# Optimization experiments

Measured on AMD Instinct MI355X. Metric: run time of the kernel, lower is better.

## Reference

```python
import jax, jax.numpy as jnp
import numpy as np

B, N, H, STEPS, IN_DIM, OUT_DIM = 512, 81, 128, 16, 10, 9
LN_EPS = 1e-5


def _build_edges():
    # Sudoku constraint graph: edge (j -> i) if cells share row, col, or 3x3 box.
    edges = []
    for i in range(81):
        ri, ci = divmod(i, 9)
        bi = ri // 3 * 3 + ci // 3
        for j in range(81):
            if i == j:
                continue
            rj, cj = divmod(j, 9)
            bj = rj // 3 * 3 + cj // 3
            if ri == rj or ci == cj or bi == bj:
                edges.append((j, i))
    e = np.asarray(edges, dtype=np.int32).T  # [2, 1620]
    return e[0], e[1]


def setup_inputs() -> dict:
    key = jax.random.key(0)
    ks = jax.random.split(key, 24)
    s = 0.02

    def w(k, shape):
        return jax.random.normal(k, shape, dtype=jnp.float32) * s

    src_np, dst_np = _build_edges()
    inp = {
        "x": jax.random.normal(ks[0], (B, N, IN_DIM), dtype=jnp.float32),
        "src": jnp.asarray(src_np),
        "dst": jnp.asarray(dst_np),
        "W_in": w(ks[1], (IN_DIM, H)), "b_in": jnp.zeros((H,), jnp.float32),
        "pos": w(ks[2], (N, H)),
        # message MLP: (2H -> H -> H -> H -> H), ReLU between
        "mW0": w(ks[3], (2 * H, H)), "mb0": jnp.zeros((H,), jnp.float32),
        "mW1": w(ks[4], (H, H)), "mb1": jnp.zeros((H,), jnp.float32),
        "mW2": w(ks[5], (H, H)), "mb2": jnp.zeros((H,), jnp.float32),
        "mW3": w(ks[6], (H, H)), "mb3": jnp.zeros((H,), jnp.float32),
        # node MLP: (3H -> H -> H -> H -> H)
        "nW0": w(ks[7], (3 * H, H)), "nb0": jnp.zeros((H,), jnp.float32),
        "nW1": w(ks[8], (H, H)), "nb1": jnp.zeros((H,), jnp.float32),
        "nW2": w(ks[9], (H, H)), "nb2": jnp.zeros((H,), jnp.float32),
        "nW3": w(ks[10], (H, H)), "nb3": jnp.zeros((H,), jnp.float32),
        "ln_g": jnp.ones((H,), jnp.float32), "ln_b": jnp.zeros((H,), jnp.float32),
        "W_out": w(ks[11], (H, OUT_DIM)), "b_out": jnp.zeros((OUT_DIM,), jnp.float32),
    }
    return inp


def _mlp(x, Ws, bs):
    for W, b in zip(Ws[:-1], bs[:-1]):
        x = jax.nn.relu(x @ W + b)
    return x @ Ws[-1] + bs[-1]


def _layer_norm(h, g, b):
    mu = jnp.mean(h, axis=-1, keepdims=True)
    var = jnp.mean(jnp.square(h - mu), axis=-1, keepdims=True)
    return (h - mu) * jax.lax.rsqrt(var + LN_EPS) * g + b


def reference(x, src, dst, W_in, b_in, pos,
              mW0, mb0, mW1, mb1, mW2, mb2, mW3, mb3,
              nW0, nb0, nW1, nb1, nW2, nb2, nW3, nb3,
              ln_g, ln_b, W_out, b_out):
    mWs, mbs = [mW0, mW1, mW2, mW3], [mb0, mb1, mb2, mb3]
    nWs, nbs = [nW0, nW1, nW2, nW3], [nb0, nb1, nb2, nb3]

    x_embed = x @ W_in + b_in + pos  # [B, N, H]
    h = x_embed
    for _ in range(STEPS):
        h_src = h[:, src]  # [B, E, H] gather
        h_dst = h[:, dst]
        messages = _mlp(jnp.concatenate([h_src, h_dst], axis=-1), mWs, mbs)  # [B, E, H]
        # scatter-add over dst -> [B, N, H]
        aggregated = jnp.zeros_like(h).at[:, dst, :].add(messages)
        h = h + _mlp(jnp.concatenate([h, x_embed, aggregated], axis=-1), nWs, nbs)
        h = _layer_norm(h, ln_g, ln_b)
    return h @ W_out + b_out  # [B, N, 9]
```

## Files before the change

### kernel.cpp

```cpp
#include <hip/hip_runtime.h>
#include <hip/hip_bf16.h>

typedef __bf16 bf16_t;
typedef bf16_t bf16x8 __attribute__((ext_vector_type(8)));
typedef bf16_t bf16x4 __attribute__((ext_vector_type(4)));
typedef float  f32x4  __attribute__((ext_vector_type(4)));
typedef float  f32x16 __attribute__((ext_vector_type(16)));

#define NN   81
#define BB   512
#define BN   41472
#define EE   1620

__device__ __forceinline__ int swz(int r, int k) {
    return (r << 7) + ((((k >> 3) ^ (r & 15)) << 3) | (k & 7));
}

__device__ __forceinline__ int wpack(int n, int k) {
    return ((n >> 6) << 13) + (((((k >> 5) << 2) + ((n >> 4) & 3))) << 9)
         + (((((k >> 3) & 3) << 4) + (n & 15)) << 3) + (k & 7);
}

__device__ __forceinline__ int wpack32(int n, int k) {
    return ((((k >> 4) << 2) | (n >> 5)) << 9)
         + (((((k >> 3) & 1) << 5) | (n & 31)) << 3) + (k & 7);
}

__device__ __forceinline__ unsigned pkbf(float lo, float hi) {
    unsigned a = __float_as_uint(lo) + 0x8000u;
    unsigned b = __float_as_uint(hi) + 0x8000u;
    return __builtin_amdgcn_perm(b, a, 0x07060302);
}

__device__ __forceinline__ unsigned pkbf_t(float lo, float hi) {
    return __builtin_amdgcn_perm(__float_as_uint(hi), __float_as_uint(lo), 0x07060302);
}

__device__ __forceinline__ float bflo(unsigned d) { return __uint_as_float(d << 16); }
__device__ __forceinline__ float bfhi(unsigned d) { return __uint_as_float(d & 0xffff0000u); }

__device__ __forceinline__ unsigned addrelu2(unsigned pd, unsigned qd) {
    float lo = fmaxf(bflo(pd) + bflo(qd), 0.f);
    float hi = fmaxf(bfhi(pd) + bfhi(qd), 0.f);
    return pkbf(lo, hi);
}

__device__ __forceinline__ void gemm128s(f32x4 (&acc)[4][4], const bf16_t* act,
                                         const bf16_t* __restrict__ Wp,
                                         int wm, int wn, int lane, int lrow, int q) {
    f32x4 z = {0.f, 0.f, 0.f, 0.f};
    #pragma unroll
    for (int i = 0; i < 4; i++)
        #pragma unroll
        for (int j = 0; j < 4; j++) acc[i][j] = z;
    const bf16_t* wbase = Wp + (wn << 13) + (lane << 3);
    #pragma unroll
    for (int k0 = 0; k0 < 128; k0 += 32) {
        bf16x8 af[4], wf[4];
        #pragma unroll
        for (int mt = 0; mt < 4; mt++)
            af[mt] = *(const bf16x8*)&act[swz(wm * 64 + mt * 16 + lrow, k0 + q * 8)];
        #pragma unroll
        for (int nt = 0; nt < 4; nt++)
            wf[nt] = *(const bf16x8*)(wbase + ((((k0 >> 5) << 2) + nt) << 9));
        #pragma unroll
        for (int nt = 0; nt < 4; nt++)
            #pragma unroll
            for (int mt = 0; mt < 4; mt++)
                acc[nt][mt] = __builtin_amdgcn_mfma_f32_16x16x32_bf16(wf[nt], af[mt], acc[nt][mt], 0, 0, 0);
    }
}

template<int MT>
__device__ __forceinline__ void gemm_e(f32x16 (&acc)[MT], const bf16_t* act,
                                       const bf16_t* __restrict__ W,
                                       const float* __restrict__ bias,
                                       int wid, int lane) {
    int lm = lane & 31, h = lane >> 5;
    #pragma unroll
    for (int gg = 0; gg < 4; gg++) {
        float4 b4 = *(const float4*)&bias[wid * 32 + 8 * gg + 4 * h];
        #pragma unroll
        for (int mt = 0; mt < MT; mt++) {
            acc[mt][4 * gg + 0] = b4.x; acc[mt][4 * gg + 1] = b4.y;
            acc[mt][4 * gg + 2] = b4.z; acc[mt][4 * gg + 3] = b4.w;
        }
    }
    const bf16_t* wl = W + (lane << 3);
    #pragma unroll
    for (int kk = 0; kk < 8; kk++) {
        bf16x8 wf = *(const bf16x8*)(wl + (((kk << 2) + wid) << 9));
        #pragma unroll
        for (int mt = 0; mt < MT; mt++) {
            bf16x8 af = *(const bf16x8*)&act[swz(mt * 32 + lm, kk * 16 + h * 8)];
            acc[mt] = __builtin_amdgcn_mfma_f32_32x32x16_bf16(wf, af, acc[mt], 0, 0, 0);
        }
    }
}

template<int MT>
__device__ __forceinline__ void wb_e(bf16_t* act, f32x16 (&acc)[MT], int wid, int lane) {
    int lm = lane & 31, h = lane >> 5;
    #pragma unroll
    for (int mt = 0; mt < MT; mt++)
        #pragma unroll
        for (int gg = 0; gg < 4; gg++) {
            int nb = wid * 32 + 8 * gg + 4 * h;
            int m = mt * 32 + lm;
            uint2 u;
            u.x = pkbf_t(fmaxf(acc[mt][4 * gg + 0], 0.f), fmaxf(acc[mt][4 * gg + 1], 0.f));
            u.y = pkbf_t(fmaxf(acc[mt][4 * gg + 2], 0.f), fmaxf(acc[mt][4 * gg + 3], 0.f));
            *(uint2*)&act[swz(m, nb)] = u;
        }
}

__device__ __forceinline__ void gemm32s(f32x4 (&acc)[2][2], const bf16_t* act,
                                        const bf16_t* __restrict__ Wp,
                                        int wid, int lane, int lrow, int q, bool zero) {
    if (zero) {
        f32x4 z = {0.f, 0.f, 0.f, 0.f};
        acc[0][0] = z; acc[0][1] = z; acc[1][0] = z; acc[1][1] = z;
    }
    int wn = wid >> 1, ntb = (wid & 1) << 1;
    const bf16_t* wbase = Wp + (wn << 13) + (lane << 3);
    #pragma unroll
    for (int k0 = 0; k0 < 128; k0 += 32) {
        bf16x8 af[2], wf[2];
        af[0] = *(const bf16x8*)&act[swz(lrow, k0 + q * 8)];
        af[1] = *(const bf16x8*)&act[swz(16 + lrow, k0 + q * 8)];
        wf[0] = *(const bf16x8*)(wbase + ((((k0 >> 5) << 2) + ntb) << 9));
        wf[1] = *(const bf16x8*)(wbase + ((((k0 >> 5) << 2) + ntb + 1) << 9));
        #pragma unroll
        for (int nt = 0; nt < 2; nt++)
            #pragma unroll
            for (int mt = 0; mt < 2; mt++)
                acc[nt][mt] = __builtin_amdgcn_mfma_f32_16x16x32_bf16(wf[nt], af[mt], acc[nt][mt], 0, 0, 0);
    }
}

__device__ __forceinline__ void wb32(bf16_t* act, f32x4 (&acc)[2][2], const float* __restrict__ bias,
                                     int colb, int lrow, int q) {
    #pragma unroll
    for (int nt = 0; nt < 2; nt++) {
        int nb = colb + nt * 16 + q * 4;
        float4 b4 = *(const float4*)&bias[nb];
        #pragma unroll
        for (int mt = 0; mt < 2; mt++) {
            int m = mt * 16 + lrow;
            uint2 u;
            u.x = pkbf_t(fmaxf(acc[nt][mt][0] + b4.x, 0.f), fmaxf(acc[nt][mt][1] + b4.y, 0.f));
            u.y = pkbf_t(fmaxf(acc[nt][mt][2] + b4.z, 0.f), fmaxf(acc[nt][mt][3] + b4.w, 0.f));
            *(uint2*)&act[swz(m, nb)] = u;
        }
    }
}


__global__ __launch_bounds__(256) void k_embed(const float* __restrict__ x, const float* __restrict__ W_in,
                                               const float* __restrict__ b_in, const float* __restrict__ pos,
                                               bf16_t* __restrict__ hb) {
    int idx = blockIdx.x * 256 + threadIdx.x;
    int row = idx >> 7, col = idx & 127;
    int n = row % NN;
    const float* xr = x + (size_t)row * 10;
    float s = b_in[col] + pos[n * 128 + col];
    #pragma unroll
    for (int k = 0; k < 10; k++) s += xr[k] * W_in[k * 128 + col];
    hb[idx] = (bf16_t)s;
}

struct PackArgs { const float* s[9]; };

__global__ __launch_bounds__(256) void k_pack_all(PackArgs pa, bf16_t* __restrict__ dst) {
    const int slot[9] = {0, 1, 2, 3, 4, 6, 7, 8, 9};
    int idx = blockIdx.x * 256 + threadIdx.x;
    int w = idx >> 14, r = idx & 16383;
    int n = r >> 7, k = r & 127;
    int po = (w == 2 || w == 3) ? wpack32(n, k) : wpack(n, k);
    dst[slot[w] * 16384 + po] = (bf16_t)pa.s[w][k * 128 + n];
}

__global__ __launch_bounds__(256) void k_fuse(const float* __restrict__ mW3, const float* __restrict__ nW0,
                                              bf16_t* __restrict__ Ft) {
    int idx = blockIdx.x * 256 + threadIdx.x;
    int n = idx >> 7, k = idx & 127;
    float s = 0.f;
    for (int j = 0; j < 128; j++) s += mW3[k * 128 + j] * nW0[(256 + j) * 128 + n];
    Ft[wpack(n, k)] = (bf16_t)s;
}

__global__ __launch_bounds__(128) void k_bias(const float* __restrict__ nb0, const float* __restrict__ mb3,
                                              const float* __restrict__ nW0, float* __restrict__ bfix) {
    int n = threadIdx.x;
    float s = 0.f;
    for (int j = 0; j < 128; j++) s += mb3[j] * nW0[(256 + j) * 128 + n];
    bfix[n] = nb0[n] + 20.f * s;
}

__global__ __launch_bounds__(256, 2) void k_simple3(const bf16_t* __restrict__ in,
                                                    const bf16_t* __restrict__ Wp,
                                                    const float* __restrict__ bfix,
                                                    const float* __restrict__ mb0,
                                                    bf16_t* __restrict__ C2b,
                                                    bf16_t* __restrict__ Pd,
                                                    bf16_t* __restrict__ Qd) {
    __shared__ __align__(16) bf16_t act[16384];
    int tid = threadIdx.x;
    int sel = blockIdx.x / 324, blk = blockIdx.x - sel * 324;
    size_t i0 = (size_t)blk * 128;
    int lane = tid & 63, wid = tid >> 6;
    int wm = wid >> 1, wn = wid & 1, lrow = lane & 15, q = lane >> 4;

    for (int ch = tid; ch < 2048; ch += 256) {
        int r = ch >> 4, p = ch & 15;
        *(uint4*)&act[swz(r, p << 3)] = *(const uint4*)(in + (i0 + r) * 128 + (p << 3));
    }
    __syncthreads();
    const bf16_t* W = Wp + (sel == 0 ? 9 * 16384 : (sel == 1 ? 0 : 16384));
    f32x4 acc[4][4];
    gemm128s(acc, act, W, wm, wn, lane, lrow, q);
    bf16_t* dst = (sel == 0) ? C2b : ((sel == 1) ? Pd : Qd);
    #pragma unroll
    for (int nt = 0; nt < 4; nt++) {
        int nb = wn * 64 + nt * 16 + q * 4;
        float4 b4 = (sel == 0) ? *(const float4*)&bfix[nb]
                  : (sel == 2) ? *(const float4*)&mb0[nb]
                               : make_float4(0.f, 0.f, 0.f, 0.f);
        #pragma unroll
        for (int mt = 0; mt < 4; mt++) {
            int m = wm * 64 + mt * 16 + lrow;
            uint2 u;
            u.x = pkbf(acc[nt][mt][0] + b4.x, acc[nt][mt][1] + b4.y);
            u.y = pkbf(acc[nt][mt][2] + b4.z, acc[nt][mt][3] + b4.w);
            *(uint2*)(dst + (i0 + m) * 128 + nb) = u;
        }
    }
}

__global__ __launch_bounds__(256, 4) void k_edge(const bf16_t* __restrict__ P, const bf16_t* __restrict__ Q,
                                                 const int* __restrict__ src, const bf16_t* __restrict__ Wp,
                                                 const float* __restrict__ mb1, const float* __restrict__ mb2,
                                                 bf16_t* __restrict__ SA) {
    __shared__ __align__(16) bf16_t act[16384];
    int tid = threadIdx.x;
    int g = blockIdx.x, b = blockIdx.y;
    int e0 = g * 120, n0 = g * 6;
    int nreal = (e0 + 120 <= EE) ? 120 : (EE - e0);
    int lane = tid & 63, w = tid >> 6;

    for (int ch = tid; ch < 2048; ch += 256) {
        int r = ch >> 4, p = ch & 15;
        uint4 o;
        if (r < nreal) {
            int e = e0 + r;
            int sn = src[e];
            int dn = n0 + r / 20;
            uint4 pv = *(const uint4*)(P + (((size_t)b * NN + sn) << 7) + (p << 3));
            uint4 qv = *(const uint4*)(Q + (((size_t)b * NN + dn) << 7) + (p << 3));
            o.x = addrelu2(pv.x, qv.x);
            o.y = addrelu2(pv.y, qv.y);
            o.z = addrelu2(pv.z, qv.z);
            o.w = addrelu2(pv.w, qv.w);
        } else {
            o.x = 0u; o.y = 0u; o.z = 0u; o.w = 0u;
        }
        *(uint4*)&act[swz(r, p << 3)] = o;
    }
    __syncthreads();

    if (nreal == 120) {
        f32x16 acc[4];
        gemm_e<4>(acc, act, Wp + 2 * 16384, mb1, w, lane);
        __syncthreads();
        wb_e<4>(act, acc, w, lane);
        __syncthreads();
        gemm_e<4>(acc, act, Wp + 3 * 16384, mb2, w, lane);
        __syncthreads();
        wb_e<4>(act, acc, w, lane);
        __syncthreads();
    } else {
        f32x16 acc[2];
        gemm_e<2>(acc, act, Wp + 2 * 16384, mb1, w, lane);
        __syncthreads();
        wb_e<2>(act, acc, w, lane);
        __syncthreads();
        gemm_e<2>(acc, act, Wp + 3 * 16384, mb2, w, lane);
        __syncthreads();
        wb_e<2>(act, acc, w, lane);
        __syncthreads();
    }

    if (tid < 192) {
        int j = tid >> 5;
        int sub = tid & 31;
        int rr = sub >> 1;
        int half = sub & 1;
        int nodes = nreal / 20;
        if (j < nodes) {
            float s0 = 0.f, s1 = 0.f, s2 = 0.f, s3 = 0.f, s4 = 0.f, s5 = 0.f, s6 = 0.f, s7 = 0.f;
            #pragma unroll
            for (int i = 0; i < 10; i++) {
                int m = 20 * j + half * 10 + i;
                bf16x8 v = *(const bf16x8*)&act[swz(m, rr << 3)];
                s0 += (float)v[0]; s1 += (float)v[1]; s2 += (float)v[2]; s3 += (float)v[3];
                s4 += (float)v[4]; s5 += (float)v[5]; s6 += (float)v[6]; s7 += (float)v[7];
            }
            s0 += __shfl_xor(s0, 1); s1 += __shfl_xor(s1, 1);
            s2 += __shfl_xor(s2, 1); s3 += __shfl_xor(s3, 1);
            s4 += __shfl_xor(s4, 1); s5 += __shfl_xor(s5, 1);
            s6 += __shfl_xor(s6, 1); s7 += __shfl_xor(s7, 1);
            if (half == 0) {
                uint4 o;
                o.x = pkbf(s0, s1); o.y = pkbf(s2, s3);
                o.z = pkbf(s4, s5); o.w = pkbf(s6, s7);
                *(uint4*)(SA + (((size_t)b * NN + n0 + j) << 7) + (rr << 3)) = o;
            }
        }
    }
}

__global__ __launch_bounds__(256, 6) void k_node(bf16_t* __restrict__ hb, const bf16_t* __restrict__ SA,
                                                 const bf16_t* __restrict__ C2b, const bf16_t* __restrict__ Wp,
                                                 const float* __restrict__ nb1, const float* __restrict__ nb2,
                                                 const float* __restrict__ nb3, const float* __restrict__ ln_g,
                                                 const float* __restrict__ ln_b, const float* __restrict__ mb0,
                                                 bf16_t* __restrict__ Pd, bf16_t* __restrict__ Qd) {
    __shared__ __align__(16) bf16_t act[4096];
    __shared__ __align__(16) bf16_t sab[4096];
    __shared__ float st[256];
    int tid = threadIdx.x;
    size_t i0 = (size_t)blockIdx.x * 32;
    int lane = tid & 63, wid = tid >> 6;
    int lrow = lane & 15, q = lane >> 4;
    int colb = wid * 32;

    for (int ch = tid; ch < 1024; ch += 256) {
        if (ch < 512) {
            int r = ch >> 4, p = ch & 15;
            *(uint4*)&act[swz(r, p << 3)] = *(const uint4*)(hb + (i0 + r) * 128 + (p << 3));
        } else {
            int r = (ch - 512) >> 4, p = ch & 15;
            *(uint4*)&sab[swz(r, p << 3)] = *(const uint4*)(SA + (i0 + r) * 128 + (p << 3));
        }
    }
    __syncthreads();
    f32x4 acc[2][2];
    gemm32s(acc, act, Wp + 4 * 16384, wid, lane, lrow, q, true);
    gemm32s(acc, sab, Wp + 5 * 16384, wid, lane, lrow, q, false);
    __syncthreads();
    #pragma unroll
    for (int nt = 0; nt < 2; nt++) {
        int nb = colb + nt * 16 + q * 4;
        #pragma unroll
        for (int mt = 0; mt < 2; mt++) {
            int m = mt * 16 + lrow;
            uint2 cv = *(const uint2*)(C2b + (i0 + m) * 128 + nb);
            uint2 u;
            u.x = pkbf_t(fmaxf(acc[nt][mt][0] + bflo(cv.x), 0.f), fmaxf(acc[nt][mt][1] + bfhi(cv.x), 0.f));
            u.y = pkbf_t(fmaxf(acc[nt][mt][2] + bflo(cv.y), 0.f), fmaxf(acc[nt][mt][3] + bfhi(cv.y), 0.f));
            *(uint2*)&act[swz(m, nb)] = u;
        }
    }
    __syncthreads();
    gemm32s(acc, act, Wp + 6 * 16384, wid, lane, lrow, q, true);
    __syncthreads();
    wb32(act, acc, nb1, colb, lrow, q);
    __syncthreads();
    gemm32s(acc, act, Wp + 7 * 16384, wid, lane, lrow, q, true);
    __syncthreads();
    wb32(act, acc, nb2, colb, lrow, q);
    __syncthreads();
    gemm32s(acc, act, Wp + 8 * 16384, wid, lane, lrow, q, true);

    float s1[2] = {0.f, 0.f}, s2[2] = {0.f, 0.f};
    #pragma unroll
    for (int nt = 0; nt < 2; nt++) {
        int nb = colb + nt * 16 + q * 4;
        float4 b4 = *(const float4*)&nb3[nb];
        #pragma unroll
        for (int mt = 0; mt < 2; mt++) {
            int m = mt * 16 + lrow;
            uint2 hv = *(const uint2*)(hb + (i0 + m) * 128 + nb);
            float v0 = acc[nt][mt][0] + b4.x + bflo(hv.x);
            float v1 = acc[nt][mt][1] + b4.y + bfhi(hv.x);
            float v2 = acc[nt][mt][2] + b4.z + bflo(hv.y);
            float v3 = acc[nt][mt][3] + b4.w + bfhi(hv.y);
            acc[nt][mt][0] = v0; acc[nt][mt][1] = v1;
            acc[nt][mt][2] = v2; acc[nt][mt][3] = v3;
            s1[mt] += v0 + v1 + v2 + v3;
            s2[mt] += v0 * v0 + v1 * v1 + v2 * v2 + v3 * v3;
        }
    }
    #pragma unroll
    for (int mt = 0; mt < 2; mt++) {
        float a = s1[mt], c = s2[mt];
        a += __shfl_xor(a, 16); c += __shfl_xor(c, 16);
        a += __shfl_xor(a, 32); c += __shfl_xor(c, 32);
        s1[mt] = a; s2[mt] = c;
    }
    if (q == 0) {
        #pragma unroll
        for (int mt = 0; mt < 2; mt++) {
            st[(mt * 16 + lrow) * 8 + wid * 2 + 0] = s1[mt];
            st[(mt * 16 + lrow) * 8 + wid * 2 + 1] = s2[mt];
        }
    }
    __syncthreads();
    float mu[2], rs[2];
    #pragma unroll
    for (int mt = 0; mt < 2; mt++) {
        int m = mt * 16 + lrow;
        float a = st[m * 8 + 0] + st[m * 8 + 2] + st[m * 8 + 4] + st[m * 8 + 6];
        float c = st[m * 8 + 1] + st[m * 8 + 3] + st[m * 8 + 5] + st[m * 8 + 7];
        a *= (1.f / 128.f); c *= (1.f / 128.f);
        mu[mt] = a;
        rs[mt] = rsqrtf(c - a * a + 1e-5f);
    }
    #pragma unroll
    for (int nt = 0; nt < 2; nt++) {
        int nb = colb + nt * 16 + q * 4;
        float4 g4 = *(const float4*)&ln_g[nb];
        float4 bb4 = *(const float4*)&ln_b[nb];
        #pragma unroll
        for (int mt = 0; mt < 2; mt++) {
            int m = mt * 16 + lrow;
            float o0 = (acc[nt][mt][0] - mu[mt]) * rs[mt] * g4.x + bb4.x;
            float o1 = (acc[nt][mt][1] - mu[mt]) * rs[mt] * g4.y + bb4.y;
            float o2 = (acc[nt][mt][2] - mu[mt]) * rs[mt] * g4.z + bb4.z;
            float o3 = (acc[nt][mt][3] - mu[mt]) * rs[mt] * g4.w + bb4.w;
            uint2 u;
            u.x = pkbf(o0, o1); u.y = pkbf(o2, o3);
            *(uint2*)(hb + (i0 + m) * 128 + nb) = u;
            *(uint2*)&act[swz(m, nb)] = u;
        }
    }
    __syncthreads();
    gemm32s(acc, act, Wp + 0 * 16384, wid, lane, lrow, q, true);
    #pragma unroll
    for (int nt = 0; nt < 2; nt++) {
        int nb = colb + nt * 16 + q * 4;
        #pragma unroll
        for (int mt = 0; mt < 2; mt++) {
            int m = mt * 16 + lrow;
            uint2 u;
            u.x = pkbf(acc[nt][mt][0], acc[nt][mt][1]);
            u.y = pkbf(acc[nt][mt][2], acc[nt][mt][3]);
            *(uint2*)(Pd + (i0 + m) * 128 + nb) = u;
        }
    }
    gemm32s(acc, act, Wp + 1 * 16384, wid, lane, lrow, q, true);
    #pragma unroll
    for (int nt = 0; nt < 2; nt++) {
        int nb = colb + nt * 16 + q * 4;
        float4 m4 = *(const float4*)&mb0[nb];
        #pragma unroll
        for (int mt = 0; mt < 2; mt++) {
            int m = mt * 16 + lrow;
            uint2 u;
            u.x = pkbf(acc[nt][mt][0] + m4.x, acc[nt][mt][1] + m4.y);
            u.y = pkbf(acc[nt][mt][2] + m4.z, acc[nt][mt][3] + m4.w);
            *(uint2*)(Qd + (i0 + m) * 128 + nb) = u;
        }
    }
}

__global__ __launch_bounds__(256) void k_out(const bf16_t* __restrict__ hb, const float* __restrict__ W_out,
                                             const float* __restrict__ b_out, float* __restrict__ out) {
    int idx = blockIdx.x * 256 + threadIdx.x;
    int row = idx / 9, o = idx - row * 9;
    const bf16_t* hr = hb + (size_t)row * 128;
    float s = b_out[o];
    #pragma unroll 4
    for (int k8 = 0; k8 < 16; k8++) {
        bf16x8 v = *(const bf16x8*)(hr + k8 * 8);
        int kb = k8 * 8;
        #pragma unroll
        for (int j = 0; j < 8; j++) s += (float)v[j] * W_out[(kb + j) * 9 + o];
    }
    out[idx] = s;
}

extern "C" void kernel_launch(void* const* d_in, const int* in_sizes, int n_in,
                              void* d_out, int out_size, void* d_ws, size_t ws_size,
                              hipStream_t stream) {
    const float* x    = (const float*)d_in[0];
    const int*   src  = (const int*)d_in[1];
    const float* W_in = (const float*)d_in[3];
    const float* b_in = (const float*)d_in[4];
    const float* pos  = (const float*)d_in[5];
    const float* mW0  = (const float*)d_in[6];
    const float* mb0  = (const float*)d_in[7];
    const float* mW1  = (const float*)d_in[8];
    const float* mb1  = (const float*)d_in[9];
    const float* mW2  = (const float*)d_in[10];
    const float* mb2  = (const float*)d_in[11];
    const float* mW3  = (const float*)d_in[12];
    const float* mb3  = (const float*)d_in[13];
    const float* nW0  = (const float*)d_in[14];
    const float* nb0  = (const float*)d_in[15];
    const float* nW1  = (const float*)d_in[16];
    const float* nb1  = (const float*)d_in[17];
    const float* nW2  = (const float*)d_in[18];
    const float* nb2  = (const float*)d_in[19];
    const float* nW3  = (const float*)d_in[20];
    const float* nb3  = (const float*)d_in[21];
    const float* ln_g = (const float*)d_in[22];
    const float* ln_b = (const float*)d_in[23];
    const float* W_out= (const float*)d_in[24];
    const float* b_out= (const float*)d_in[25];

    char* ws = (char*)d_ws;
    bf16_t* hb  = (bf16_t*)ws;
    bf16_t* C2b = (bf16_t*)(ws + 10616832);
    bf16_t* SA  = (bf16_t*)(ws + 21233664);
    bf16_t* P   = (bf16_t*)(ws + 31850496);
    bf16_t* Q   = (bf16_t*)(ws + 42467328);
    bf16_t* Wp  = (bf16_t*)(ws + 53084160);
    float*  bfix= (float*)(ws + 53411840);

    k_embed<<<20736, 256, 0, stream>>>(x, W_in, b_in, pos, hb);

    PackArgs pa;
    pa.s[0] = mW0;  pa.s[1] = mW0 + 16384; pa.s[2] = mW1; pa.s[3] = mW2;
    pa.s[4] = nW0;  pa.s[5] = nW1;  pa.s[6] = nW2;  pa.s[7] = nW3;  pa.s[8] = nW0 + 16384;
    k_pack_all<<<576, 256, 0, stream>>>(pa, Wp);
    k_fuse<<<64, 256, 0, stream>>>(mW3, nW0, Wp + 5 * 16384);
    k_bias<<<1, 128, 0, stream>>>(nb0, mb3, nW0, bfix);

    k_simple3<<<972, 256, 0, stream>>>(hb, Wp, bfix, mb0, C2b, P, Q);

    for (int s = 0; s < 16; s++) {
        k_edge<<<dim3(14, 512), 256, 0, stream>>>(P, Q, src, Wp, mb1, mb2, SA);
        k_node<<<1296, 256, 0, stream>>>(hb, SA, C2b, Wp, nb1, nb2, nb3, ln_g, ln_b, mb0, P, Q);
    }
    k_out<<<1458, 256, 0, stream>>>(hb, W_out, b_out, (float*)d_out);
}
```

Measured before the change: 2.155 ms.

## Split edge-MLP rows into two halves to cut accumulator registers and raise occupancy

The edge kernel now computes its 120-row tile as two 64-row halves (rows 0-59 and 64-123), holding only two 32x32 accumulators per wave instead of four. This frees registers so launch bounds can rise from 4 to 5 blocks per SIMD-group. Writeback of one half is interleaved with the GEMM of the other half between barriers. In exchange it adds padding rows, more complex row remapping in the gather and reduction, and reloads weights twice per layer.

```diff
diff --git a/kernel.cpp b/kernel.cpp
--- a/kernel.cpp
+++ b/kernel.cpp
@@ -71,17 +71,16 @@
     }
 }
 
-template<int MT>
-__device__ __forceinline__ void gemm_e(f32x16 (&acc)[MT], const bf16_t* act,
-                                       const bf16_t* __restrict__ W,
-                                       const float* __restrict__ bias,
-                                       int wid, int lane) {
+__device__ __forceinline__ void gemm_eh(f32x16 (&acc)[2], const bf16_t* act,
+                                        const bf16_t* __restrict__ W,
+                                        const float* __restrict__ bias,
+                                        int wid, int lane, int mbase) {
     int lm = lane & 31, h = lane >> 5;
     #pragma unroll
     for (int gg = 0; gg < 4; gg++) {
         float4 b4 = *(const float4*)&bias[wid * 32 + 8 * gg + 4 * h];
         #pragma unroll
-        for (int mt = 0; mt < MT; mt++) {
+        for (int mt = 0; mt < 2; mt++) {
             acc[mt][4 * gg + 0] = b4.x; acc[mt][4 * gg + 1] = b4.y;
             acc[mt][4 * gg + 2] = b4.z; acc[mt][4 * gg + 3] = b4.w;
         }
@@ -91,22 +90,21 @@
     for (int kk = 0; kk < 8; kk++) {
         bf16x8 wf = *(const bf16x8*)(wl + (((kk << 2) + wid) << 9));
         #pragma unroll
-        for (int mt = 0; mt < MT; mt++) {
-            bf16x8 af = *(const bf16x8*)&act[swz(mt * 32 + lm, kk * 16 + h * 8)];
+        for (int mt = 0; mt < 2; mt++) {
+            bf16x8 af = *(const bf16x8*)&act[swz(mbase + mt * 32 + lm, kk * 16 + h * 8)];
             acc[mt] = __builtin_amdgcn_mfma_f32_32x32x16_bf16(wf, af, acc[mt], 0, 0, 0);
         }
     }
 }
 
-template<int MT>
-__device__ __forceinline__ void wb_e(bf16_t* act, f32x16 (&acc)[MT], int wid, int lane) {
+__device__ __forceinline__ void wb_eh(bf16_t* act, f32x16 (&acc)[2], int wid, int lane, int mbase) {
     int lm = lane & 31, h = lane >> 5;
     #pragma unroll
-    for (int mt = 0; mt < MT; mt++)
+    for (int mt = 0; mt < 2; mt++)
         #pragma unroll
         for (int gg = 0; gg < 4; gg++) {
             int nb = wid * 32 + 8 * gg + 4 * h;
-            int m = mt * 32 + lm;
+            int m = mbase + mt * 32 + lm;
             uint2 u;
             u.x = pkbf_t(fmaxf(acc[mt][4 * gg + 0], 0.f), fmaxf(acc[mt][4 * gg + 1], 0.f));
             u.y = pkbf_t(fmaxf(acc[mt][4 * gg + 2], 0.f), fmaxf(acc[mt][4 * gg + 3], 0.f));
@@ -237,7 +235,7 @@
     }
 }
 
-__global__ __launch_bounds__(256, 4) void k_edge(const bf16_t* __restrict__ P, const bf16_t* __restrict__ Q,
+__global__ __launch_bounds__(256, 5) void k_edge(const bf16_t* __restrict__ P, const bf16_t* __restrict__ Q,
                                                  const int* __restrict__ src, const bf16_t* __restrict__ Wp,
                                                  const float* __restrict__ mb1, const float* __restrict__ mb2,
                                                  bf16_t* __restrict__ SA) {
@@ -247,14 +245,16 @@
     int e0 = g * 120, n0 = g * 6;
     int nreal = (e0 + 120 <= EE) ? 120 : (EE - e0);
     int lane = tid & 63, w = tid >> 6;
+    bool two = (nreal == 120);
 
     for (int ch = tid; ch < 2048; ch += 256) {
         int r = ch >> 4, p = ch & 15;
+        int e = (r < 64) ? r : r - 4;
+        bool real = (r < 60 || r >= 64) && (e < nreal) && (r < 124);
         uint4 o;
-        if (r < nreal) {
-            int e = e0 + r;
-            int sn = src[e];
-            int dn = n0 + r / 20;
+        if (real) {
+            int sn = src[e0 + e];
+            int dn = n0 + e / 20;
             uint4 pv = *(const uint4*)(P + (((size_t)b * NN + sn) << 7) + (p << 3));
             uint4 qv = *(const uint4*)(Q + (((size_t)b * NN + dn) << 7) + (p << 3));
             o.x = addrelu2(pv.x, qv.x);
@@ -268,27 +268,20 @@
     }
     __syncthreads();
 
-    if (nreal == 120) {
-        f32x16 acc[4];
-        gemm_e<4>(acc, act, Wp + 2 * 16384, mb1, w, lane);
-        __syncthreads();
-        wb_e<4>(act, acc, w, lane);
-        __syncthreads();
-        gemm_e<4>(acc, act, Wp + 3 * 16384, mb2, w, lane);
-        __syncthreads();
-        wb_e<4>(act, acc, w, lane);
-        __syncthreads();
-    } else {
-        f32x16 acc[2];
-        gemm_e<2>(acc, act, Wp + 2 * 16384, mb1, w, lane);
-        __syncthreads();
-        wb_e<2>(act, acc, w, lane);
-        __syncthreads();
-        gemm_e<2>(acc, act, Wp + 3 * 16384, mb2, w, lane);
-        __syncthreads();
-        wb_e<2>(act, acc, w, lane);
-        __syncthreads();
-    }
+    f32x16 acc[2];
+    gemm_eh(acc, act, Wp + 2 * 16384, mb1, w, lane, 0);
+    __syncthreads();
+    wb_eh(act, acc, w, lane, 0);
+    if (two) gemm_eh(acc, act, Wp + 2 * 16384, mb1, w, lane, 64);
+    __syncthreads();
+    if (two) wb_eh(act, acc, w, lane, 64);
+    gemm_eh(acc, act, Wp + 3 * 16384, mb2, w, lane, 0);
+    __syncthreads();
+    wb_eh(act, acc, w, lane, 0);
+    if (two) gemm_eh(acc, act, Wp + 3 * 16384, mb2, w, lane, 64);
+    __syncthreads();
+    if (two) wb_eh(act, acc, w, lane, 64);
+    __syncthreads();
 
     if (tid < 192) {
         int j = tid >> 5;
@@ -297,10 +290,11 @@
         int half = sub & 1;
         int nodes = nreal / 20;
         if (j < nodes) {
+            int rb = (j < 3) ? j * 20 : 64 + (j - 3) * 20;
             float s0 = 0.f, s1 = 0.f, s2 = 0.f, s3 = 0.f, s4 = 0.f, s5 = 0.f, s6 = 0.f, s7 = 0.f;
             #pragma unroll
             for (int i = 0; i < 10; i++) {
-                int m = 20 * j + half * 10 + i;
+                int m = rb + half * 10 + i;
                 bf16x8 v = *(const bf16x8*)&act[swz(m, rr << 3)];
                 s0 += (float)v[0]; s1 += (float)v[1]; s2 += (float)v[2]; s3 += (float)v[3];
                 s4 += (float)v[4]; s5 += (float)v[5]; s6 += (float)v[6]; s7 += (float)v[7];
```

New measurement: 2.382 ms. 10.5% more time.
